# Optimization experiments

Hardware: AMD Instinct MI355X
Metric: run time of the kernel (lower is better)

## Reference

```python
import jax, jax.numpy as jnp
import numpy as np

WSZ = 2
ZNEAR, ZFAR = 0.1, 100.0


def _grid_sample_bilinear(img, gx, gy):
    # img [H,W]; gx,gy [n] normalized coords in [-1,1]
    # matches torch F.grid_sample(mode='bilinear', padding_mode='zeros', align_corners=True)
    H, W = img.shape
    ix = (gx + 1.0) * 0.5 * (W - 1)
    iy = (gy + 1.0) * 0.5 * (H - 1)
    x0 = jnp.floor(ix)
    y0 = jnp.floor(iy)
    wx = ix - x0
    wy = iy - y0
    x0i = x0.astype(jnp.int32)
    y0i = y0.astype(jnp.int32)

    def tap(xi, yi):
        v = (xi >= 0) & (xi < W) & (yi >= 0) & (yi < H)
        return img[jnp.clip(yi, 0, H - 1), jnp.clip(xi, 0, W - 1)] * v

    return (tap(x0i, y0i) * (1 - wx) * (1 - wy)
            + tap(x0i + 1, y0i) * wx * (1 - wy)
            + tap(x0i, y0i + 1) * (1 - wx) * wy
            + tap(x0i + 1, y0i + 1) * wx * wy)


def _forward(alpha, beta, pp, conf, pose_w2c, K):
    b, _, n = pp.shape
    h, w = alpha.shape[-2:]
    H2, W2 = h * WSZ, w * WSZ

    # project points: pc = pose_w2c @ pp[:, :4]
    pc = jnp.einsum('bij,bjn->bin', pose_w2c, pp[:, :4])  # [b,4,n]
    z = jnp.abs(pc[:, 2])
    xc = pc[:, 0] * K[:, 0, 0][:, None] / z + K[:, 0, 2][:, None]
    yc = pc[:, 1] * K[:, 1, 1][:, None] / z + K[:, 1, 2][:, None]

    gx = xc / float(w - 1) * 2.0 - 1.0
    gy = -(yc / float(h - 1) * 2.0 - 1.0)
    conf_sampled = jax.vmap(_grid_sample_bilinear)(beta[:, 0], gx, gy)[:, None]  # [b,1,n]

    xs = jnp.round(xc * WSZ).astype(jnp.int32)
    ys = jnp.round(yc * WSZ).astype(jnp.int32)
    oob = ((xs < 0) | (xs >= W2) | (ys < 0) | (ys >= H2)
           | (z < ZNEAR) | (z > ZFAR) | (conf <= 0))
    valid = ~oob

    alpha_up = jnp.repeat(jnp.repeat(alpha[:, 0], WSZ, axis=-1), WSZ, axis=-2)[:, ::-1, :]

    idx_pts = jnp.arange(n, dtype=jnp.int32)
    row_base = jnp.arange(h)[:, None] * WSZ
    col_base = jnp.arange(w)[None, :] * WSZ

    def one(conf_b, xs_b, ys_b, valid_b, alpha_b):
        # scatter conf / point-index into hi-res z-buffer (invalid -> dropped)
        flat = jnp.where(valid_b, ys_b * W2 + xs_b, H2 * W2)
        cmap = jnp.zeros(H2 * W2, conf_b.dtype).at[flat].set(conf_b, mode='drop').reshape(H2, W2)
        idxh = jnp.full(H2 * W2, -1, jnp.int32).at[flat].set(idx_pts, mode='drop').reshape(H2, W2)
        keep = (alpha_b > 0) & (cmap > 0)
        cm = cmap * keep
        # 2x2 max-pool with indices
        win = cm.reshape(h, WSZ, w, WSZ).transpose(0, 2, 1, 3).reshape(h, w, WSZ * WSZ)
        a = jnp.argmax(win, axis=-1)  # [h,w] in 0..3
        rows = row_base + a // WSZ
        cols = col_base + a % WSZ
        idxh = jnp.where(keep, idxh, -1)
        idx_sel = idxh[rows, cols]
        match = keep.astype(cm.dtype).reshape(h, WSZ, w, WSZ).max(axis=(1, 3))
        return match[::-1], idx_sel[::-1]

    match, midx = jax.vmap(one)(conf, xs, ys, valid, alpha_up)
    return match[:, None], midx[:, None], conf_sampled


def setup_inputs() -> dict:
    key = jax.random.key(0)
    ks = jax.random.split(key, 8)
    b, h, w = 8, 480, 640
    n = h * w
    fx = fy = 500.0
    cx, cy = (w - 1) / 2.0, (h - 1) / 2.0
    # back-project uniformly sampled pixels/depths -> geometrically valid cloud
    u = jax.random.uniform(ks[0], (b, n), minval=0.0, maxval=w - 1.0)
    v = jax.random.uniform(ks[1], (b, n), minval=0.0, maxval=h - 1.0)
    zz = jax.random.uniform(ks[2], (b, n), minval=0.5, maxval=10.0)
    X = (u - cx) * zz / fx
    Y = (v - cy) * zz / fy
    rgb = jax.random.uniform(ks[3], (b, 3, n))
    pp = jnp.concatenate([jnp.stack([X, Y, zz, jnp.ones_like(zz)], axis=1), rgb], axis=1).astype(jnp.float32)
    pose_w2c = jnp.tile(jnp.eye(4, dtype=jnp.float32), (b, 1, 1))
    K = jnp.tile(jnp.array([[fx, 0.0, cx], [0.0, fy, cy], [0.0, 0.0, 1.0]], jnp.float32), (b, 1, 1))
    alpha = (jax.random.uniform(ks[4], (b, 1, h, w)) > 0.05).astype(jnp.float32)
    beta = jax.random.uniform(ks[5], (b, 1, h, w))
    conf = jax.random.uniform(ks[6], (b, n), minval=-0.1, maxval=1.0)
    return {"alpha": alpha, "beta": beta, "pp": pp, "conf": conf,
            "pose_w2c": pose_w2c, "K": K, "h": h, "w": w}


def reference(alpha, beta, pp, conf, pose_w2c, K, h, w):
    # h, w are ignored by the original module (re-read from alpha)
    return _forward(alpha, beta, pp, conf, pose_w2c, K)
```

## Files before the change

kernel.cpp:

```cpp
#include <hip/hip_runtime.h>

#define WSZ 2
#define ZNEAR 0.1f
#define ZFAR 100.0f
#define NT 256
#define CHUNK 2048
#define KPT (CHUNK / NT)
#define GRP 4
#define CELLSZ 6144
#define THIST 256
#define CSTRIDE 16

__device__ __forceinline__ void derive_geom(int h, int w, int n,
                                            int& H2, int& W2, int& rpt,
                                            int& cpt, int& tpb, bool& ok) {
    H2 = h * WSZ; W2 = w * WSZ;
    rpt = (H2 + THIST - 1) / THIST;
    rpt = (rpt + 1) & ~1;
    if (rpt < 2) rpt = 2;
    cpt = rpt * W2;
    tpb = (H2 + rpt - 1) / rpt;
    ok = (cpt <= CELLSZ) && (tpb <= THIST) && (n <= (1 << 19)) && (cpt <= 8192);
}

__global__ void __launch_bounds__(NT)
project_bin_kernel(const float* __restrict__ pp,
                   const float* __restrict__ conf,
                   const float* __restrict__ pose,
                   const float* __restrict__ Kmat,
                   const float* __restrict__ beta,
                   const int* __restrict__ d_h,
                   const int* __restrict__ d_w,
                   int* __restrict__ counters,
                   unsigned int* __restrict__ records,
                   float* __restrict__ out_conf,
                   int n, int b, int cap) {
    __shared__ unsigned int staging[CHUNK];
    __shared__ int hist[THIST];
    __shared__ int segstart[THIST];
    __shared__ int cursor[THIST];
    __shared__ int gbase[THIST];
    __shared__ int wsum[NT / 64];
    __shared__ int tot_s;

    const int h = *d_h, w = *d_w;
    int H2, W2, rpt, cpt, tpb; bool geom_ok;
    derive_geom(h, w, n, H2, W2, rpt, cpt, tpb, geom_ok);

    const int b_idx = blockIdx.x % b;
    const int off   = (blockIdx.x / b) * CHUNK;
    const int tid   = threadIdx.x;

    hist[tid] = 0;
    __syncthreads();

    const float* P  = pose + b_idx * 16;
    const float* Kb = Kmat + b_idx * 9;
    const float fxk = Kb[0], cxk = Kb[2], fyk = Kb[4], cyk = Kb[5];
    const float p00 = P[0], p01 = P[1], p02 = P[2],  p03 = P[3];
    const float p10 = P[4], p11 = P[5], p12 = P[6],  p13 = P[7];
    const float p20 = P[8], p21 = P[9], p22 = P[10], p23 = P[11];
    const float* B = beta + (size_t)b_idx * h * w;

    unsigned int words[KPT];
    #pragma unroll
    for (int k = 0; k < KPT; ++k) words[k] = 0xFFFFFFFFu;

    #pragma unroll
    for (int g = 0; g < KPT; g += GRP) {
        float xc_[GRP], yc_[GRP], z_[GRP], cf_[GRP], ix_[GRP], iy_[GRP];
        bool act_[GRP], sok_[GRP];

        #pragma unroll
        for (int q = 0; q < GRP; ++q) {
            int k = g + q;
            int i = off + k * NT + tid;
            bool act = (i < n);
            act_[q] = act;
            float px = 0.f, py = 0.f, pz = 0.f, pw = 0.f, cf = 0.f;
            if (act) {
                const float* ppb = pp + (size_t)b_idx * 7 * n + i;
                px = __builtin_nontemporal_load(ppb);
                py = __builtin_nontemporal_load(ppb + (size_t)n);
                pz = __builtin_nontemporal_load(ppb + (size_t)2 * n);
                pw = __builtin_nontemporal_load(ppb + (size_t)3 * n);
                cf = conf[(size_t)b_idx * n + i];
            }
            float pc0 = p00 * px + p01 * py + p02 * pz + p03 * pw;
            float pc1 = p10 * px + p11 * py + p12 * pz + p13 * pw;
            float pc2 = p20 * px + p21 * py + p22 * pz + p23 * pw;
            float z = fabsf(pc2);
            float xc = pc0 * fxk / z + cxk;
            float yc = pc1 * fyk / z + cyk;
            float gx = xc / (float)(w - 1) * 2.0f - 1.0f;
            float gy = -(yc / (float)(h - 1) * 2.0f - 1.0f);
            float ix = (gx + 1.0f) * 0.5f * (float)(w - 1);
            float iy = (gy + 1.0f) * 0.5f * (float)(h - 1);
            xc_[q] = xc; yc_[q] = yc; z_[q] = z; cf_[q] = cf;
            ix_[q] = ix; iy_[q] = iy;
            sok_[q] = act && (ix > -1.0f) && (ix < (float)w)
                          && (iy > -1.0f) && (iy < (float)h);
        }

        float t00[GRP], t10[GRP], t01[GRP], t11[GRP];
        #pragma unroll
        for (int q = 0; q < GRP; ++q) {
            t00[q] = t10[q] = t01[q] = t11[q] = 0.0f;
            if (!sok_[q]) continue;
            int x0 = (int)floorf(ix_[q]);
            int y0 = (int)floorf(iy_[q]);
            bool pair = (x0 >= 0) && (x0 + 1 < w) && ((x0 & 1) == 0);
            if (y0 >= 0 && y0 < h) {
                const float* R = B + (size_t)y0 * w;
                if (pair) {
                    float2 p2 = *reinterpret_cast<const float2*>(R + x0);
                    t00[q] = p2.x; t10[q] = p2.y;
                } else {
                    if (x0 >= 0 && x0 < w)         t00[q] = R[x0];
                    if (x0 + 1 >= 0 && x0 + 1 < w) t10[q] = R[x0 + 1];
                }
            }
            if (y0 + 1 >= 0 && y0 + 1 < h) {
                const float* R = B + (size_t)(y0 + 1) * w;
                if (pair) {
                    float2 p2 = *reinterpret_cast<const float2*>(R + x0);
                    t01[q] = p2.x; t11[q] = p2.y;
                } else {
                    if (x0 >= 0 && x0 < w)         t01[q] = R[x0];
                    if (x0 + 1 >= 0 && x0 + 1 < w) t11[q] = R[x0 + 1];
                }
            }
        }

        #pragma unroll
        for (int q = 0; q < GRP; ++q) {
            int k = g + q;
            int i = off + k * NT + tid;
            if (!act_[q]) continue;
            float cs = 0.0f;
            if (sok_[q]) {
                float x0f = floorf(ix_[q]), y0f = floorf(iy_[q]);
                float wx = ix_[q] - x0f, wy = iy_[q] - y0f;
                cs = t00[q] * (1.0f - wx) * (1.0f - wy)
                   + t10[q] * wx * (1.0f - wy)
                   + t01[q] * (1.0f - wx) * wy
                   + t11[q] * wx * wy;
            }
            __builtin_nontemporal_store(cs, out_conf + (size_t)b_idx * n + i);

            float rx = rintf(xc_[q] * (float)WSZ);
            float ry = rintf(yc_[q] * (float)WSZ);
            bool valid = (rx >= 0.0f) && (rx < (float)W2) &&
                         (ry >= 0.0f) && (ry < (float)H2) &&
                         (z_[q] >= ZNEAR) && (z_[q] <= ZFAR) && (cf_[q] > 0.0f);
            if (valid && geom_ok) {
                int xs = (int)rx, ys = (int)ry;
                int ty = (int)((unsigned)ys / (unsigned)rpt);
                int cib = (ys - ty * rpt) * W2 + xs;
                words[k] = ((unsigned)ty << 13) | (unsigned)cib;
                atomicAdd(&hist[ty], 1);
            }
        }
    }
    __syncthreads();

    const int lane = tid & 63, wv = tid >> 6;
    int own = hist[tid];
    int v = own;
    #pragma unroll
    for (int s = 1; s < 64; s <<= 1) {
        int u = __shfl_up(v, s, 64);
        if (lane >= s) v += u;
    }
    if (lane == 63) wsum[wv] = v;
    __syncthreads();
    int basew = 0;
    #pragma unroll
    for (int t = 0; t < NT / 64; ++t)
        if (t < wv) basew += wsum[t];
    int incl = basew + v;
    int sstart = incl - own;
    segstart[tid] = sstart;
    cursor[tid] = sstart;
    if (tid == NT - 1) tot_s = incl;
    gbase[tid] = (tid < tpb && own > 0)
               ? atomicAdd(&counters[(b_idx * tpb + tid) * CSTRIDE], own) : 0;
    __syncthreads();

    #pragma unroll
    for (int k = 0; k < KPT; ++k) {
        unsigned int word = words[k];
        if (word == 0xFFFFFFFFu) continue;
        int ty = (int)(word >> 13);
        unsigned int cib = word & 8191u;
        int i = off + k * NT + tid;
        int slot = atomicAdd(&cursor[ty], 1);
        staging[slot] = (cib << 19) | (unsigned)i;
    }
    __syncthreads();

    const int tot = tot_s;
    for (int j = tid; j < tot; j += NT) {
        int lo = 0, hi = THIST - 1;
        while (lo < hi) {
            int mid = (lo + hi + 1) >> 1;
            if (segstart[mid] <= j) lo = mid; else hi = mid - 1;
        }
        int t = lo;
        int gpos = gbase[t] + (j - segstart[t]);
        if (gpos < cap)
            records[(size_t)(b_idx * tpb + t) * cap + gpos] = staging[j];
    }
}

__global__ void __launch_bounds__(NT)
pool_bins_kernel(const float* __restrict__ alpha,
                 const float* __restrict__ conf,
                 const int* __restrict__ counters,
                 const unsigned int* __restrict__ records,
                 const int* __restrict__ d_h,
                 const int* __restrict__ d_w,
                 float* __restrict__ out_match,
                 float* __restrict__ out_midx,
                 int b, int n, int hw, int cap) {
    __shared__ int cells[CELLSZ];
    const int h = *d_h, w = *d_w;
    int H2, W2, rpt, cpt, tpb; bool geom_ok;
    derive_geom(h, w, n, H2, W2, rpt, cpt, tpb, geom_ok);
    if (!geom_ok) return;

    const int b_idx = blockIdx.x % b;
    const int ty    = blockIdx.x / b;
    if (ty >= tpb) return;
    const int bin = b_idx * tpb + ty;

    for (int i = threadIdx.x; i < cpt; i += NT) cells[i] = -1;
    __syncthreads();

    int cnt = counters[bin * CSTRIDE];
    if (cnt > cap) cnt = cap;
    const unsigned int* rec = records + (size_t)bin * cap;
    for (int r = threadIdx.x; r < cnt; r += NT) {
        unsigned int rr = rec[r];
        atomicMax(&cells[rr >> 19], (int)(rr & 0x7FFFFu));
    }
    __syncthreads();

    const int row0 = ty * rpt;
    int rmax = H2 - row0; if (rmax > rpt) rmax = rpt;
    const float* A = alpha + (size_t)b_idx * hw;
    const float* C = conf + (size_t)b_idx * n;

    for (int q = 0; q < rmax / 2; ++q) {
        int hr = (row0 >> 1) + q;
        int r_out = h - 1 - hr;
        for (int c = threadIdx.x; c < w; c += NT) {
            float av = A[r_out * w + c];
            float best = 0.0f;
            int besti = -1;
            if (av > 0.0f) {
                #pragma unroll
                for (int a = 0; a < 4; ++a) {
                    int dy = a >> 1, dx = a & 1;
                    int widx = cells[(2 * q + dy) * W2 + 2 * c + dx];
                    if (widx >= 0) {
                        float cv = C[widx];
                        if (cv > best) { best = cv; besti = widx; }
                    }
                }
            }
            int o = b_idx * hw + r_out * w + c;
            out_match[o] = (best > 0.0f) ? 1.0f : 0.0f;
            out_midx[o]  = (float)besti;
        }
    }
}

extern "C" void kernel_launch(void* const* d_in, const int* in_sizes, int n_in,
                              void* d_out, int out_size, void* d_ws, size_t ws_size,
                              hipStream_t stream) {
    const float* alpha = (const float*)d_in[0];
    const float* beta  = (const float*)d_in[1];
    const float* pp    = (const float*)d_in[2];
    const float* conf  = (const float*)d_in[3];
    const float* pose  = (const float*)d_in[4];
    const float* Kmat  = (const float*)d_in[5];
    const int*   d_h   = (const int*)d_in[6];
    const int*   d_w   = (const int*)d_in[7];

    const int b  = in_sizes[4] / 16;
    const int n  = in_sizes[3] / b;
    const int hw = in_sizes[0] / b;

    float* out_match = (float*)d_out;
    float* out_midx  = out_match + (size_t)b * hw;
    float* out_conf  = out_midx + (size_t)b * hw;

    const int nb_ub = b * THIST;

    long avail_ints = (long)(ws_size / 4) - (long)nb_ub * CSTRIDE;
    long cap_l = avail_ints / (nb_ub > 0 ? nb_ub : 1);
    int cap = (int)cap_l;
    if (cap > 4096) cap = 4096;
    if (cap < 64) cap = 64;

    int* counters = (int*)d_ws;
    unsigned int* records = (unsigned int*)(counters + (size_t)nb_ub * CSTRIDE);

    hipMemsetAsync(counters, 0, (size_t)nb_ub * CSTRIDE * sizeof(int), stream);

    const int bpb = (n + CHUNK - 1) / CHUNK;
    project_bin_kernel<<<b * bpb, NT, 0, stream>>>(
        pp, conf, pose, Kmat, beta, d_h, d_w,
        counters, records, out_conf, n, b, cap);

    pool_bins_kernel<<<nb_ub, NT, 0, stream>>>(
        alpha, conf, counters, records, d_h, d_w,
        out_match, out_midx, b, n, hw, cap);
}
```

Baseline: 85.58 us.

## Move bilinear beta sampling into bin pooling kernel using shared-memory staged rows

Adds a new project/pool kernel pair. The projection kernel now stores projected xc/yc to workspace and skips the beta gather. The pooling kernel stages the relevant beta rows for its row band into shared memory and does the bilinear sample per binned point there. Points that fall outside the sampling window are zeroed early, and invalid-but-in-window points are binned with a sentinel cell so their confidence still gets computed. This aims to replace scattered global beta reads with LDS reads, at the cost of extra workspace traffic for xcyc and more records per bin. The old path is kept as a fallback when workspace is too small.

```diff
diff --git a/kernel.cpp b/kernel.cpp
--- a/kernel.cpp
+++ b/kernel.cpp
@@ -8,8 +8,10 @@
 #define KPT (CHUNK / NT)
 #define GRP 4
 #define CELLSZ 6144
+#define BSTAGE 3072
 #define THIST 256
 #define CSTRIDE 16
+#define SENT 8191u
 
 __device__ __forceinline__ void derive_geom(int h, int w, int n,
                                             int& H2, int& W2, int& rpt,
@@ -20,20 +22,282 @@
     if (rpt < 2) rpt = 2;
     cpt = rpt * W2;
     tpb = (H2 + rpt - 1) / rpt;
-    ok = (cpt <= CELLSZ) && (tpb <= THIST) && (n <= (1 << 19)) && (cpt <= 8192);
+    ok = (cpt <= CELLSZ) && (tpb <= THIST) && (n <= (1 << 19)) && (cpt < (int)SENT)
+         && ((rpt / 2 + 2) * w <= BSTAGE);
 }
 
+
 __global__ void __launch_bounds__(NT)
-project_bin_kernel(const float* __restrict__ pp,
-                   const float* __restrict__ conf,
-                   const float* __restrict__ pose,
-                   const float* __restrict__ Kmat,
-                   const float* __restrict__ beta,
-                   const int* __restrict__ d_h,
-                   const int* __restrict__ d_w,
-                   int* __restrict__ counters,
-                   unsigned int* __restrict__ records,
-                   float* __restrict__ out_conf,
+project_bin2_kernel(const float* __restrict__ pp,
+                    const float* __restrict__ conf,
+                    const float* __restrict__ pose,
+                    const float* __restrict__ Kmat,
+                    const int* __restrict__ d_h,
+                    const int* __restrict__ d_w,
+                    int* __restrict__ counters,
+                    unsigned int* __restrict__ records,
+                    float* __restrict__ xcyc,
+                    float* __restrict__ out_conf,
+                    int n, int b, int cap) {
+    __shared__ unsigned int staging[CHUNK];
+    __shared__ int hist[THIST];
+    __shared__ int segstart[THIST];
+    __shared__ int cursor[THIST];
+    __shared__ int gbase[THIST];
+    __shared__ int wsum[NT / 64];
+    __shared__ int tot_s;
+
+    const int h = *d_h, w = *d_w;
+    int H2, W2, rpt, cpt, tpb; bool geom_ok;
+    derive_geom(h, w, n, H2, W2, rpt, cpt, tpb, geom_ok);
+
+    const int b_idx = blockIdx.x % b;
+    const int off   = (blockIdx.x / b) * CHUNK;
+    const int tid   = threadIdx.x;
+
+    hist[tid] = 0;
+    __syncthreads();
+
+    const float* P  = pose + b_idx * 16;
+    const float* Kb = Kmat + b_idx * 9;
+    const float fxk = Kb[0], cxk = Kb[2], fyk = Kb[4], cyk = Kb[5];
+    const float p00 = P[0], p01 = P[1], p02 = P[2],  p03 = P[3];
+    const float p10 = P[4], p11 = P[5], p12 = P[6],  p13 = P[7];
+    const float p20 = P[8], p21 = P[9], p22 = P[10], p23 = P[11];
+
+    unsigned int words[KPT];
+    #pragma unroll
+    for (int k = 0; k < KPT; ++k) words[k] = 0xFFFFFFFFu;
+
+    #pragma unroll
+    for (int g = 0; g < KPT; g += GRP) {
+        float xc_[GRP], yc_[GRP], z_[GRP], cf_[GRP];
+        bool act_[GRP];
+
+        #pragma unroll
+        for (int q = 0; q < GRP; ++q) {
+            int k = g + q;
+            int i = off + k * NT + tid;
+            bool act = (i < n);
+            act_[q] = act;
+            float px = 0.f, py = 0.f, pz = 0.f, pw = 0.f, cf = 0.f;
+            if (act) {
+                const float* ppb = pp + (size_t)b_idx * 7 * n + i;
+                px = __builtin_nontemporal_load(ppb);
+                py = __builtin_nontemporal_load(ppb + (size_t)n);
+                pz = __builtin_nontemporal_load(ppb + (size_t)2 * n);
+                pw = __builtin_nontemporal_load(ppb + (size_t)3 * n);
+                cf = conf[(size_t)b_idx * n + i];
+            }
+            float pc0 = p00 * px + p01 * py + p02 * pz + p03 * pw;
+            float pc1 = p10 * px + p11 * py + p12 * pz + p13 * pw;
+            float pc2 = p20 * px + p21 * py + p22 * pz + p23 * pw;
+            float z = fabsf(pc2);
+            xc_[q] = pc0 * fxk / z + cxk;
+            yc_[q] = pc1 * fyk / z + cyk;
+            z_[q] = z; cf_[q] = cf;
+        }
+
+        #pragma unroll
+        for (int q = 0; q < GRP; ++q) {
+            int k = g + q;
+            int i = off + k * NT + tid;
+            if (!act_[q]) continue;
+            size_t gidx = (size_t)b_idx * n + i;
+            float xc = xc_[q], yc = yc_[q];
+            __builtin_nontemporal_store(xc, xcyc + 2 * gidx);
+            __builtin_nontemporal_store(yc, xcyc + 2 * gidx + 1);
+
+            float gx = xc / (float)(w - 1) * 2.0f - 1.0f;
+            float gy = -(yc / (float)(h - 1) * 2.0f - 1.0f);
+            float ix = (gx + 1.0f) * 0.5f * (float)(w - 1);
+            float iy = (gy + 1.0f) * 0.5f * (float)(h - 1);
+            bool sok = (ix > -1.0f) && (ix < (float)w)
+                    && (iy > -1.0f) && (iy < (float)h);
+
+            if (!sok || !geom_ok) {
+                __builtin_nontemporal_store(0.0f, out_conf + gidx);
+                continue;
+            }
+            float rx = rintf(xc * (float)WSZ);
+            float ry = rintf(yc * (float)WSZ);
+            bool valid = (rx >= 0.0f) && (rx < (float)W2) &&
+                         (ry >= 0.0f) && (ry < (float)H2) &&
+                         (z_[q] >= ZNEAR) && (z_[q] <= ZFAR) && (cf_[q] > 0.0f);
+            int ys_cl = min(max((int)ry, 0), H2 - 1);
+            int ty = ys_cl / rpt;
+            unsigned int cib = SENT;
+            if (valid) cib = (unsigned)(((int)ry - ty * rpt) * W2 + (int)rx);
+            words[k] = ((unsigned)ty << 13) | cib;
+            atomicAdd(&hist[ty], 1);
+        }
+    }
+    __syncthreads();
+
+    const int lane = tid & 63, wv = tid >> 6;
+    int own = hist[tid];
+    int v = own;
+    #pragma unroll
+    for (int s = 1; s < 64; s <<= 1) {
+        int u = __shfl_up(v, s, 64);
+        if (lane >= s) v += u;
+    }
+    if (lane == 63) wsum[wv] = v;
+    __syncthreads();
+    int basew = 0;
+    #pragma unroll
+    for (int t = 0; t < NT / 64; ++t)
+        if (t < wv) basew += wsum[t];
+    int incl = basew + v;
+    int sstart = incl - own;
+    segstart[tid] = sstart;
+    cursor[tid] = sstart;
+    if (tid == NT - 1) tot_s = incl;
+    gbase[tid] = (tid < tpb && own > 0)
+               ? atomicAdd(&counters[(b_idx * THIST + tid) * CSTRIDE], own) : 0;
+    __syncthreads();
+
+    #pragma unroll
+    for (int k = 0; k < KPT; ++k) {
+        unsigned int word = words[k];
+        if (word == 0xFFFFFFFFu) continue;
+        int ty = (int)(word >> 13);
+        unsigned int cib = word & 8191u;
+        int i = off + k * NT + tid;
+        int slot = atomicAdd(&cursor[ty], 1);
+        staging[slot] = (cib << 19) | (unsigned)i;
+    }
+    __syncthreads();
+
+    const int tot = tot_s;
+    for (int j = tid; j < tot; j += NT) {
+        int lo = 0, hi = THIST - 1;
+        while (lo < hi) {
+            int mid = (lo + hi + 1) >> 1;
+            if (segstart[mid] <= j) lo = mid; else hi = mid - 1;
+        }
+        int t = lo;
+        int gpos = gbase[t] + (j - segstart[t]);
+        if (gpos < cap)
+            records[(size_t)(b_idx * THIST + t) * cap + gpos] = staging[j];
+    }
+}
+
+__global__ void __launch_bounds__(NT)
+pool_bins2_kernel(const float* __restrict__ alpha,
+                  const float* __restrict__ beta,
+                  const float* __restrict__ conf,
+                  const int* __restrict__ counters,
+                  const unsigned int* __restrict__ records,
+                  const float* __restrict__ xcyc,
+                  const int* __restrict__ d_h,
+                  const int* __restrict__ d_w,
+                  float* __restrict__ out_match,
+                  float* __restrict__ out_midx,
+                  float* __restrict__ out_conf,
+                  int b, int n, int hw, int cap) {
+    __shared__ int cells[CELLSZ];
+    __shared__ float betar[BSTAGE];
+    const int h = *d_h, w = *d_w;
+    int H2, W2, rpt, cpt, tpb; bool geom_ok;
+    derive_geom(h, w, n, H2, W2, rpt, cpt, tpb, geom_ok);
+    if (!geom_ok) return;
+
+    const int b_idx = blockIdx.x % b;
+    const int ty    = blockIdx.x / b;
+    if (ty >= tpb) return;
+    const int bin = b_idx * THIST + ty;
+    const int tid = threadIdx.x;
+
+    const int nrows = rpt / 2 + 2;
+    const int base = h - 1 - (rpt / 2) * ty - rpt / 2;
+
+    for (int i = tid; i < cpt; i += NT) cells[i] = -1;
+    const float* B = beta + (size_t)b_idx * hw;
+    for (int r = 0; r < nrows; ++r) {
+        int row = base + r;
+        if (row >= 0 && row < h)
+            for (int x = tid; x < w; x += NT)
+                betar[r * w + x] = B[(size_t)row * w + x];
+    }
+    __syncthreads();
+
+    int cnt = counters[bin * CSTRIDE];
+    if (cnt > cap) cnt = cap;
+    const unsigned int* rec = records + (size_t)bin * cap;
+    const float* XY = xcyc + (size_t)b_idx * n * 2;
+
+    for (int r = tid; r < cnt; r += NT) {
+        unsigned int rr = rec[r];
+        int i = (int)(rr & 0x7FFFFu);
+        unsigned int cib = rr >> 19;
+        float xc = XY[2 * i];
+        float yc = XY[2 * i + 1];
+        float gx = xc / (float)(w - 1) * 2.0f - 1.0f;
+        float gy = -(yc / (float)(h - 1) * 2.0f - 1.0f);
+        float ix = (gx + 1.0f) * 0.5f * (float)(w - 1);
+        float iy = (gy + 1.0f) * 0.5f * (float)(h - 1);
+        float x0f = floorf(ix), y0f = floorf(iy);
+        float wx = ix - x0f, wy = iy - y0f;
+        int x0 = (int)x0f, y0 = (int)y0f;
+        int xi0 = min(max(x0, 0), w - 1);
+        int xi1 = min(max(x0 + 1, 0), w - 1);
+        bool mx0 = (x0 >= 0);
+        bool mx1 = (x0 + 1 < w);
+        int r0 = min(max(y0 - base, 0), nrows - 1);
+        int r1 = min(max(y0 + 1 - base, 0), nrows - 1);
+        bool my0 = (y0 >= 0) && (y0 < h);
+        bool my1 = (y0 + 1 >= 0) && (y0 + 1 < h);
+        float t00 = (mx0 && my0) ? betar[r0 * w + xi0] : 0.0f;
+        float t10 = (mx1 && my0) ? betar[r0 * w + xi1] : 0.0f;
+        float t01 = (mx0 && my1) ? betar[r1 * w + xi0] : 0.0f;
+        float t11 = (mx1 && my1) ? betar[r1 * w + xi1] : 0.0f;
+        float cs = t00 * (1.0f - wx) * (1.0f - wy)
+                 + t10 * wx * (1.0f - wy)
+                 + t01 * (1.0f - wx) * wy
+                 + t11 * wx * wy;
+        out_conf[(size_t)b_idx * n + i] = cs;
+        if (cib != SENT) atomicMax(&cells[cib], i);
+    }
+    __syncthreads();
+
+    const int row0 = ty * rpt;
+    int rmax = H2 - row0; if (rmax > rpt) rmax = rpt;
+    const float* A = alpha + (size_t)b_idx * hw;
+    const float* C = conf + (size_t)b_idx * n;
+
+    for (int q = 0; q < rmax / 2; ++q) {
+        int hr = (row0 >> 1) + q;
+        int r_out = h - 1 - hr;
+        for (int c = tid; c < w; c += NT) {
+            float av = A[r_out * w + c];
+            float best = 0.0f;
+            int besti = -1;
+            if (av > 0.0f) {
+                #pragma unroll
+                for (int a = 0; a < 4; ++a) {
+                    int dy = a >> 1, dx = a & 1;
+                    int widx = cells[(2 * q + dy) * W2 + 2 * c + dx];
+                    if (widx >= 0) {
+                        float cv = C[widx];
+                        if (cv > best) { best = cv; besti = widx; }
+                    }
+                }
+            }
+            int o = b_idx * hw + r_out * w + c;
+            out_match[o] = (best > 0.0f) ? 1.0f : 0.0f;
+            out_midx[o]  = (float)besti;
+        }
+    }
+}
+
+
+__global__ void __launch_bounds__(NT)
+project_bin_kernel(const float* __restrict__ pp, const float* __restrict__ conf,
+                   const float* __restrict__ pose, const float* __restrict__ Kmat,
+                   const float* __restrict__ beta, const int* __restrict__ d_h,
+                   const int* __restrict__ d_w, int* __restrict__ counters,
+                   unsigned int* __restrict__ records, float* __restrict__ out_conf,
                    int n, int b, int cap) {
     __shared__ unsigned int staging[CHUNK];
     __shared__ int hist[THIST];
@@ -184,7 +448,7 @@
     cursor[tid] = sstart;
     if (tid == NT - 1) tot_s = incl;
     gbase[tid] = (tid < tpb && own > 0)
-               ? atomicAdd(&counters[(b_idx * tpb + tid) * CSTRIDE], own) : 0;
+               ? atomicAdd(&counters[(b_idx * THIST + tid) * CSTRIDE], own) : 0;
     __syncthreads();
 
     #pragma unroll
@@ -209,19 +473,15 @@
         int t = lo;
         int gpos = gbase[t] + (j - segstart[t]);
         if (gpos < cap)
-            records[(size_t)(b_idx * tpb + t) * cap + gpos] = staging[j];
+            records[(size_t)(b_idx * THIST + t) * cap + gpos] = staging[j];
     }
 }
 
 __global__ void __launch_bounds__(NT)
-pool_bins_kernel(const float* __restrict__ alpha,
-                 const float* __restrict__ conf,
-                 const int* __restrict__ counters,
-                 const unsigned int* __restrict__ records,
-                 const int* __restrict__ d_h,
-                 const int* __restrict__ d_w,
-                 float* __restrict__ out_match,
-                 float* __restrict__ out_midx,
+pool_bins_kernel(const float* __restrict__ alpha, const float* __restrict__ conf,
+                 const int* __restrict__ counters, const unsigned int* __restrict__ records,
+                 const int* __restrict__ d_h, const int* __restrict__ d_w,
+                 float* __restrict__ out_match, float* __restrict__ out_midx,
                  int b, int n, int hw, int cap) {
     __shared__ int cells[CELLSZ];
     const int h = *d_h, w = *d_w;
@@ -232,7 +492,7 @@
     const int b_idx = blockIdx.x % b;
     const int ty    = blockIdx.x / b;
     if (ty >= tpb) return;
-    const int bin = b_idx * tpb + ty;
+    const int bin = b_idx * THIST + ty;
 
     for (int i = threadIdx.x; i < cpt; i += NT) cells[i] = -1;
     __syncthreads();
@@ -276,6 +536,7 @@
     }
 }
 
+
 extern "C" void kernel_launch(void* const* d_in, const int* in_sizes, int n_in,
                               void* d_out, int out_size, void* d_ws, size_t ws_size,
                               hipStream_t stream) {
@@ -291,30 +552,51 @@
     const int b  = in_sizes[4] / 16;
     const int n  = in_sizes[3] / b;
     const int hw = in_sizes[0] / b;
+    const long total = (long)b * n;
 
     float* out_match = (float*)d_out;
     float* out_midx  = out_match + (size_t)b * hw;
     float* out_conf  = out_midx + (size_t)b * hw;
 
     const int nb_ub = b * THIST;
-
-    long avail_ints = (long)(ws_size / 4) - (long)nb_ub * CSTRIDE;
-    long cap_l = avail_ints / (nb_ub > 0 ? nb_ub : 1);
-    int cap = (int)cap_l;
-    if (cap > 4096) cap = 4096;
-    if (cap < 64) cap = 64;
-
-    int* counters = (int*)d_ws;
-    unsigned int* records = (unsigned int*)(counters + (size_t)nb_ub * CSTRIDE);
-
-    hipMemsetAsync(counters, 0, (size_t)nb_ub * CSTRIDE * sizeof(int), stream);
-
+    const long cnt_ints = (long)nb_ub * CSTRIDE;
     const int bpb = (n + CHUNK - 1) / CHUNK;
-    project_bin_kernel<<<b * bpb, NT, 0, stream>>>(
-        pp, conf, pose, Kmat, beta, d_h, d_w,
-        counters, records, out_conf, n, b, cap);
-
-    pool_bins_kernel<<<nb_ub, NT, 0, stream>>>(
-        alpha, conf, counters, records, d_h, d_w,
-        out_match, out_midx, b, n, hw, cap);
+
+    long cap_new_l = ((long)(ws_size / 4) - cnt_ints - 2 * total) / nb_ub;
+    if (cap_new_l > 4096) cap_new_l = 4096;
+
+    if (cap_new_l >= 1792) {
+        int cap = (int)cap_new_l;
+        int* counters = (int*)d_ws;
+        float* xcyc = (float*)(counters + cnt_ints);
+        unsigned int* records = (unsigned int*)(xcyc + 2 * total);
+
+        hipMemsetAsync(counters, 0, cnt_ints * sizeof(int), stream);
+
+        project_bin2_kernel<<<b * bpb, NT, 0, stream>>>(
+            pp, conf, pose, Kmat, d_h, d_w,
+            counters, records, xcyc, out_conf, n, b, cap);
+
+        pool_bins2_kernel<<<nb_ub, NT, 0, stream>>>(
+            alpha, beta, conf, counters, records, xcyc, d_h, d_w,
+            out_match, out_midx, out_conf, b, n, hw, cap);
+    } else {
+        long cap_l = ((long)(ws_size / 4) - cnt_ints) / nb_ub;
+        int cap = (int)cap_l;
+        if (cap > 4096) cap = 4096;
+        if (cap < 64) cap = 64;
+
+        int* counters = (int*)d_ws;
+        unsigned int* records = (unsigned int*)(counters + cnt_ints);
+
+        hipMemsetAsync(counters, 0, cnt_ints * sizeof(int), stream);
+
+        project_bin_kernel<<<b * bpb, NT, 0, stream>>>(
+            pp, conf, pose, Kmat, beta, d_h, d_w,
+            counters, records, out_conf, n, b, cap);
+
+        pool_bins_kernel<<<nb_ub, NT, 0, stream>>>(
+            alpha, conf, counters, records, d_h, d_w,
+            out_match, out_midx, b, n, hw, cap);
+    }
 }
```

Result: slower. 93.97 us (+9.8%).
